# Performance work log

Measured on AMD Instinct MI355X. Metric: run time of the kernel, lower is better.

The kernel has to match this reference:

```python
import jax, jax.numpy as jnp
import numpy as np

N = 40000      # nodes
E = 640000     # edges
D = 128        # in_dim == hidden_dim
G = 64         # graphs in batch
L = 3          # n_layers
EPS = 1e-5     # BatchNorm eps


def setup_inputs() -> dict:
    key = jax.random.key(0)
    ks = jax.random.split(key, 8)
    x = jax.random.normal(ks[0], (N, D), dtype=jnp.float32)
    edge_index = jax.random.randint(ks[1], (2, E), 0, N, dtype=jnp.int64)
    batch = jnp.sort(jax.random.randint(ks[2], (N,), 0, G, dtype=jnp.int64))
    Ws = jax.random.normal(ks[3], (L, D, D), dtype=jnp.float32) * 0.05
    bs = jnp.zeros((L, D), jnp.float32)
    gammas = jnp.ones((L, D), jnp.float32)
    betas = jnp.zeros((L, D), jnp.float32)
    w1 = jax.random.normal(ks[4], (D, D // 2), dtype=jnp.float32) * 0.05
    b1 = jnp.zeros((D // 2,), jnp.float32)
    w2 = jax.random.normal(ks[5], (D // 2, 1), dtype=jnp.float32) * 0.05
    b2 = jnp.zeros((1,), jnp.float32)
    return {"x": x, "edge_index": edge_index, "batch": batch, "Ws": Ws,
            "bs": bs, "gammas": gammas, "betas": betas,
            "w1": w1, "b1": b1, "w2": w2, "b2": b2}


def reference(x, edge_index, batch, Ws, bs, gammas, betas, w1, b1, w2, b2):
    # GCNConv (PyG default): add self-loops, symmetric D^-1/2 (A+I) D^-1/2 norm
    loops = jnp.arange(N, dtype=edge_index.dtype)
    src = jnp.concatenate([edge_index[0], loops])  # [E+N]
    dst = jnp.concatenate([edge_index[1], loops])  # [E+N]
    deg = jax.ops.segment_sum(jnp.ones_like(dst, dtype=x.dtype), dst, num_segments=N)
    dinv = jnp.where(deg > 0, jax.lax.rsqrt(deg), 0.0)
    norm = (dinv[src] * dinv[dst])[:, None]        # [E+N, 1]

    h = x
    for l in range(L):
        h = h @ Ws[l] + bs[l]                                  # linear transform
        h = jax.ops.segment_sum(h[src] * norm, dst, num_segments=N)  # scatter-add agg
        h = jax.nn.relu(h)
        # BatchNorm1d (training-mode batch statistics, biased var)
        mean = h.mean(axis=0)
        var = h.var(axis=0)
        h = gammas[l] * (h - mean) * jax.lax.rsqrt(var + EPS) + betas[l]
        # dropout p=0.0 -> identity

    # global_mean_pool over graph ids
    counts = jax.ops.segment_sum(jnp.ones((N,), h.dtype), batch, num_segments=G)
    pooled = jax.ops.segment_sum(h, batch, num_segments=G) / jnp.maximum(counts, 1.0)[:, None]

    out = jax.nn.relu(pooled @ w1 + b1) @ w2 + b2
    return out.squeeze(-1)  # [G]
```

## Files before the change

kernel.cpp:

```cpp
#include <hip/hip_runtime.h>
#include <hip/hip_fp16.h>

#define N_NODES 40000
#define N_EDGES 640000
#define DIM 128
#define N_GRAPHS 64
#define BN_EPS 1e-5f
#define AGG_BLOCKS 2048
#define SCAN_NB 40
#define GEMM_NB (N_NODES / 64)
#define WTP 136

typedef _Float16 f16x8 __attribute__((ext_vector_type(8)));
typedef float    f32x4 __attribute__((ext_vector_type(4)));

__global__ __launch_bounds__(256) void k_count_edges(const int* __restrict__ ei, int* __restrict__ cnt,
                                                     int* __restrict__ rank) {
    int e = blockIdx.x * 256 + threadIdx.x;
    if (e < N_EDGES) rank[e] = atomicAdd(&cnt[ei[N_EDGES + e]], 1);
}

__global__ __launch_bounds__(1024) void k_scan_blk(const int* __restrict__ cnt, int* __restrict__ off,
                                                   int* __restrict__ blocksum) {
    __shared__ int sums[1024];
    int i = blockIdx.x * 1024 + threadIdx.x;
    int v = (i < N_NODES) ? cnt[i] : 0;
    sums[threadIdx.x] = v;
    __syncthreads();
    for (int d = 1; d < 1024; d <<= 1) {
        int t = (threadIdx.x >= d) ? sums[threadIdx.x - d] : 0;
        __syncthreads();
        sums[threadIdx.x] += t;
        __syncthreads();
    }
    if (i < N_NODES) off[i] = sums[threadIdx.x] - v;
    if (threadIdx.x == 1023) blocksum[blockIdx.x] = sums[1023];
}

__global__ __launch_bounds__(1024) void k_scan_fix(const int* __restrict__ cnt, const int* __restrict__ blocksum,
                                                   int* __restrict__ off, float* __restrict__ dinv,
                                                   const int* __restrict__ batch, int* __restrict__ goff) {
    __shared__ int bo[2];
    if (threadIdx.x == 0) {
        int run = 0, tot = 0;
        for (int b = 0; b < SCAN_NB; ++b) {
            int v = blocksum[b];
            if (b < (int)blockIdx.x) run += v;
            tot += v;
        }
        bo[0] = run; bo[1] = tot;
    }
    __syncthreads();
    int i = blockIdx.x * 1024 + threadIdx.x;
    if (i < N_NODES) {
        off[i] += bo[0];
        dinv[i] = rsqrtf((float)(cnt[i] + 1));
        int b = batch[i];
        int bp = (i == 0) ? -1 : batch[i - 1];
        for (int g = bp + 1; g <= b; ++g) goff[g] = i;
        if (i == N_NODES - 1)
            for (int g = b + 1; g <= N_GRAPHS; ++g) goff[g] = N_NODES;
    }
    if (i == 0) off[N_NODES] = bo[1];
}

__global__ __launch_bounds__(256) void k_fill(const int* __restrict__ ei, const int* __restrict__ rank,
                                              const int* __restrict__ off, int* __restrict__ elist) {
    int e = blockIdx.x * 256 + threadIdx.x;
    if (e < N_EDGES) {
        int s = ei[e];
        int d = ei[N_EDGES + e];
        elist[off[d] + rank[e]] = s;
    }
}

__global__ __launch_bounds__(256) void k_prepw(const float* __restrict__ Ws, __half* __restrict__ wt) {
    int idx = blockIdx.x * 256 + threadIdx.x;
    if (idx >= 3 * DIM * DIM) return;
    int l = idx >> 14;
    int rem = idx & 16383;
    int k = rem >> 7;
    int c = rem & 127;
    float w = Ws[(size_t)l * DIM * DIM + k * DIM + c];
    __half hi = __float2half(w);
    __half lo = __float2half(w - __half2float(hi));
    size_t base = (size_t)l * 2 * DIM * WTP;
    wt[base + (size_t)c * WTP + k] = hi;
    wt[base + (size_t)DIM * WTP + (size_t)c * WTP + k] = lo;
}

__device__ __forceinline__ void gemm_core(const __half* __restrict__ wt2, const float* __restrict__ bias,
                                          __half* __restrict__ out16, __half* Wl2, __half* Al,
                                          int t, long row0) {
    {
        const float4* src = (const float4*)wt2;
        float4* dst = (float4*)Wl2;
        for (int i = t; i < 4352; i += 256) dst[i] = src[i];
    }
    __syncthreads();

    int w = t >> 6;
    int l = t & 63;
    int lr = l & 15;
    int lk = (l >> 4) * 8;

    f32x4 acc[8];
#pragma unroll
    for (int i = 0; i < 8; ++i) acc[i] = (f32x4)(0.f);

#pragma unroll
    for (int ks = 0; ks < 4; ++ks) {
        f16x8 a = *(const f16x8*)&Al[(w * 16 + lr) * WTP + ks * 32 + lk];
#pragma unroll
        for (int tile = 0; tile < 8; ++tile) {
            f16x8 bh = *(const f16x8*)&Wl2[(tile * 16 + lr) * WTP + ks * 32 + lk];
            f16x8 bl = *(const f16x8*)&Wl2[DIM * WTP + (tile * 16 + lr) * WTP + ks * 32 + lk];
            acc[tile] = __builtin_amdgcn_mfma_f32_16x16x32_f16(a, bh, acc[tile], 0, 0, 0);
            acc[tile] = __builtin_amdgcn_mfma_f32_16x16x32_f16(a, bl, acc[tile], 0, 0, 0);
        }
    }

    long orow = row0 + w * 16 + (l >> 4) * 4;
#pragma unroll
    for (int tile = 0; tile < 8; ++tile) {
        int col = tile * 16 + lr;
        float b = bias[col];
#pragma unroll
        for (int i = 0; i < 4; ++i)
            out16[(orow + i) * DIM + col] = __float2half(acc[tile][i] + b);
    }
}

__global__ __launch_bounds__(256) void k_gemm_f32(const float* __restrict__ in, const __half* __restrict__ wt2,
                                                  const float* __restrict__ bias, __half* __restrict__ out16) {
    __shared__ __half Wl2[2 * DIM * WTP];
    __shared__ __half Al[64 * WTP];
    int t = threadIdx.x;
    long row0 = (long)blockIdx.x * 64;
    for (int i = t; i < 2048; i += 256) {
        int r = i >> 5, k4 = i & 31;
        float4 v = ((const float4*)(in + (row0 + r) * DIM))[k4];
        __half2* d = (__half2*)&Al[r * WTP + k4 * 4];
        d[0] = __floats2half2_rn(v.x, v.y);
        d[1] = __floats2half2_rn(v.z, v.w);
    }
    gemm_core(wt2, bias, out16, Wl2, Al, t, row0);
}

__global__ __launch_bounds__(256) void k_gemm_f16(const __half* __restrict__ in, const __half* __restrict__ wt2,
                                                  const float* __restrict__ bias, const float* __restrict__ ac,
                                                  __half* __restrict__ out16) {
    __shared__ __half Wl2[2 * DIM * WTP];
    __shared__ __half Al[64 * WTP];
    int t = threadIdx.x;
    long row0 = (long)blockIdx.x * 64;
    for (int i = t; i < 1024; i += 256) {
        int r = i >> 4, k8 = i & 15;
        const __half2* src = (const __half2*)(in + (row0 + r) * DIM + k8 * 8);
        int k = k8 * 8;
        float2 f0 = __half22float2(src[0]);
        float2 f1 = __half22float2(src[1]);
        float2 f2 = __half22float2(src[2]);
        float2 f3 = __half22float2(src[3]);
        f0.x = fmaf(ac[k + 0], f0.x, ac[DIM + k + 0]); f0.y = fmaf(ac[k + 1], f0.y, ac[DIM + k + 1]);
        f1.x = fmaf(ac[k + 2], f1.x, ac[DIM + k + 2]); f1.y = fmaf(ac[k + 3], f1.y, ac[DIM + k + 3]);
        f2.x = fmaf(ac[k + 4], f2.x, ac[DIM + k + 4]); f2.y = fmaf(ac[k + 5], f2.y, ac[DIM + k + 5]);
        f3.x = fmaf(ac[k + 6], f3.x, ac[DIM + k + 6]); f3.y = fmaf(ac[k + 7], f3.y, ac[DIM + k + 7]);
        __half2* d = (__half2*)&Al[r * WTP + k];
        d[0] = __floats2half2_rn(f0.x, f0.y);
        d[1] = __floats2half2_rn(f1.x, f1.y);
        d[2] = __floats2half2_rn(f2.x, f2.y);
        d[3] = __floats2half2_rn(f3.x, f3.y);
    }
    gemm_core(wt2, bias, out16, Wl2, Al, t, row0);
}

__global__ __launch_bounds__(256) void k_agg(const __half* __restrict__ h16, const int* __restrict__ off,
                                             const int* __restrict__ elist,
                                             const float* __restrict__ dinv, __half* __restrict__ hout,
                                             float* __restrict__ partials) {
    __shared__ float colacc[256];
    colacc[threadIdx.x] = 0.f;
    __syncthreads();

    const __half2* rows = (const __half2*)h16;
    int lane = threadIdx.x & 63;
    int wid = (blockIdx.x * 256 + threadIdx.x) >> 6;
    const int NW = AGG_BLOCKS * 4;
    float s0 = 0.f, s1 = 0.f, q0 = 0.f, q1 = 0.f;

    for (int i = wid; i < N_NODES; i += NW) {
        float di = dinv[i];
        float selfc = di * di;
        float2 rv = __half22float2(rows[(long)i * 64 + lane]);
        float a0 = rv.x * selfc, a1 = rv.y * selfc;
        int e  = off[i];
        int e1 = off[i + 1];
#pragma unroll 4
        for (; e < e1; ++e) {
            int s = elist[e];
            float c = dinv[s] * di;
            float2 r = __half22float2(rows[(long)s * 64 + lane]);
            a0 = fmaf(r.x, c, a0);
            a1 = fmaf(r.y, c, a1);
        }
        a0 = fmaxf(a0, 0.f);
        a1 = fmaxf(a1, 0.f);
        ((__half2*)(hout + (long)i * DIM))[lane] = __floats2half2_rn(a0, a1);
        s0 += a0; q0 += a0 * a0; s1 += a1; q1 += a1 * a1;
    }

    atomicAdd(&colacc[2 * lane],           s0);
    atomicAdd(&colacc[2 * lane + 1],       s1);
    atomicAdd(&colacc[128 + 2 * lane],     q0);
    atomicAdd(&colacc[128 + 2 * lane + 1], q1);
    __syncthreads();
    partials[(long)blockIdx.x * 256 + threadIdx.x] = colacc[threadIdx.x];
}

__global__ __launch_bounds__(1024) void k_stats(const float* __restrict__ partials,
                                                const float* __restrict__ gamma, const float* __restrict__ beta,
                                                float* __restrict__ ac) {
    __shared__ float ls[1024], lq[1024];
    int dd = threadIdx.x & 15;
    int seg = threadIdx.x >> 4;
    int d = blockIdx.x * 16 + dd;
    float s = 0.f, q = 0.f;
    for (int b = seg; b < AGG_BLOCKS; b += 64) {
        s += partials[b * 256 + d];
        q += partials[b * 256 + 128 + d];
    }
    ls[threadIdx.x] = s; lq[threadIdx.x] = q;
    __syncthreads();
    for (int off = 512; off >= 16; off >>= 1) {
        if (threadIdx.x < off) {
            ls[threadIdx.x] += ls[threadIdx.x + off];
            lq[threadIdx.x] += lq[threadIdx.x + off];
        }
        __syncthreads();
    }
    if (threadIdx.x < 16) {
        s = ls[threadIdx.x]; q = lq[threadIdx.x];
        float mean = s * (1.f / N_NODES);
        float var  = q * (1.f / N_NODES) - mean * mean;
        float a = gamma[d] * rsqrtf(var + BN_EPS);
        ac[d] = a;
        ac[DIM + d] = fmaf(-mean, a, beta[d]);
    }
}

__global__ __launch_bounds__(1024) void k_pool(const __half* __restrict__ h, const float* __restrict__ ac,
                                               const int* __restrict__ goff, float* __restrict__ pooled) {
    __shared__ float2 red[1024];
    int g = blockIdx.x;
    int d2 = threadIdx.x & 63;
    int seg = threadIdx.x >> 6;
    int r0 = goff[g], r1 = goff[g + 1];
    const __half2* rows = (const __half2*)h;
    float s0 = 0.f, s1 = 0.f;
    for (int r = r0 + seg; r < r1; r += 16) {
        float2 v = __half22float2(rows[(long)r * 64 + d2]);
        s0 += v.x; s1 += v.y;
    }
    red[threadIdx.x] = make_float2(s0, s1);
    __syncthreads();
    for (int off = 512; off >= 64; off >>= 1) {
        if (threadIdx.x < off) {
            red[threadIdx.x].x += red[threadIdx.x + off].x;
            red[threadIdx.x].y += red[threadIdx.x + off].y;
        }
        __syncthreads();
    }
    if (threadIdx.x < 64) {
        float2 s = red[threadIdx.x];
        int n = r1 - r0;
        float fn = (float)n;
        float denom = (float)(n > 0 ? n : 1);
        int d = 2 * threadIdx.x;
        pooled[g * DIM + d]     = (ac[d] * s.x     + ac[DIM + d] * fn)     / denom;
        pooled[g * DIM + d + 1] = (ac[d + 1] * s.y + ac[DIM + d + 1] * fn) / denom;
    }
}

__global__ __launch_bounds__(64) void k_mlp(const float* __restrict__ pooled, const float* __restrict__ w1,
                                            const float* __restrict__ b1, const float* __restrict__ w2,
                                            const float* __restrict__ b2, float* __restrict__ out) {
    int g = blockIdx.x, j = threadIdx.x;
    const float* p = pooled + g * DIM;
    float h = b1[j];
#pragma unroll
    for (int k = 0; k < DIM; ++k) h = fmaf(p[k], w1[k * 64 + j], h);
    h = fmaxf(h, 0.f);
    float v = h * w2[j];
#pragma unroll
    for (int o = 32; o > 0; o >>= 1) v += __shfl_down(v, o);
    if (j == 0) out[g] = v + b2[0];
}

extern "C" void kernel_launch(void* const* d_in, const int* in_sizes, int n_in,
                              void* d_out, int out_size, void* d_ws, size_t ws_size,
                              hipStream_t stream) {
    const float* x      = (const float*)d_in[0];
    const int*   ei     = (const int*)d_in[1];
    const int*   batch  = (const int*)d_in[2];
    const float* Ws     = (const float*)d_in[3];
    const float* bs     = (const float*)d_in[4];
    const float* gammas = (const float*)d_in[5];
    const float* betas  = (const float*)d_in[6];
    const float* w1     = (const float*)d_in[7];
    const float* b1     = (const float*)d_in[8];
    const float* w2     = (const float*)d_in[9];
    const float* b2     = (const float*)d_in[10];
    float* out = (float*)d_out;

    char* p = (char*)d_ws;
    auto alloc = [&](size_t bytes) { void* r = (void*)p; p += (bytes + 255) & ~(size_t)255; return r; };
    int*    cnt      = (int*)alloc((size_t)N_NODES * 4);
    int*    off      = (int*)alloc((size_t)(N_NODES + 1) * 4);
    int*    rank     = (int*)alloc((size_t)N_EDGES * 4);
    int*    goff     = (int*)alloc((size_t)(N_GRAPHS + 1) * 4);
    int*    blocksum = (int*)alloc((size_t)(SCAN_NB + 1) * 4);
    int*    elist    = (int*)alloc((size_t)N_EDGES * 4);
    float*  dinv     = (float*)alloc((size_t)N_NODES * 4);
    __half* wt       = (__half*)alloc((size_t)3 * 2 * DIM * WTP * 2);
    __half* h16      = (__half*)alloc((size_t)N_NODES * DIM * 2);
    __half* v16      = (__half*)alloc((size_t)N_NODES * DIM * 2);
    float*  parts    = (float*)alloc((size_t)AGG_BLOCKS * 256 * 4);
    float*  ac       = (float*)alloc(256 * 4);
    float*  pooled   = (float*)alloc((size_t)N_GRAPHS * DIM * 4);

    hipMemsetAsync(cnt, 0, (size_t)N_NODES * 4, stream);

    k_count_edges<<<(N_EDGES + 255) / 256, 256, 0, stream>>>(ei, cnt, rank);
    k_scan_blk<<<SCAN_NB, 1024, 0, stream>>>(cnt, off, blocksum);
    k_scan_fix<<<SCAN_NB, 1024, 0, stream>>>(cnt, blocksum, off, dinv, batch, goff);
    k_fill<<<(N_EDGES + 255) / 256, 256, 0, stream>>>(ei, rank, off, elist);
    k_prepw<<<(3 * DIM * DIM + 255) / 256, 256, 0, stream>>>(Ws, wt);

    for (int l = 0; l < 3; ++l) {
        if (l == 0)
            k_gemm_f32<<<GEMM_NB, 256, 0, stream>>>(x, wt, bs, h16);
        else
            k_gemm_f16<<<GEMM_NB, 256, 0, stream>>>(v16, wt + (size_t)l * 2 * DIM * WTP,
                                                    bs + (size_t)l * DIM, ac, h16);
        k_agg<<<AGG_BLOCKS, 256, 0, stream>>>(h16, off, elist, dinv, v16, parts);
        k_stats<<<8, 1024, 0, stream>>>(parts, gammas + (size_t)l * DIM, betas + (size_t)l * DIM, ac);
    }
    k_pool<<<N_GRAPHS, 1024, 0, stream>>>(v16, ac, goff, pooled);
    k_mlp<<<N_GRAPHS, 64, 0, stream>>>(pooled, w1, b1, w2, b2, out);
}
```

Baseline: 276.3 us.

## Make GEMM persistent with double-buffered A tiles and fuse pool with MLP

The GEMM kernels become persistent: 256 blocks each load the split-fp16 weight matrix into LDS once and loop over 64-row tiles. The next A tile is staged into a second LDS buffer while MFMA runs on the current one. This amortizes the 70KB weight copy per block and overlaps global loads with compute, at the cost of more LDS per block (lower occupancy) and fewer blocks than the 256 CUs might prefer. Separately, the pooling and MLP head are fused into one kernel, which removes a launch and the pooled buffer round trip.

After: 260.4 us. 5.7% less time.

```diff
diff --git a/kernel.cpp b/kernel.cpp
--- a/kernel.cpp
+++ b/kernel.cpp
@@ -8,7 +8,8 @@
 #define BN_EPS 1e-5f
 #define AGG_BLOCKS 2048
 #define SCAN_NB 40
-#define GEMM_NB (N_NODES / 64)
+#define NTILES 625
+#define GEMM_BLOCKS 256
 #define WTP 136
 
 typedef _Float16 f16x8 __attribute__((ext_vector_type(8)));
@@ -89,54 +90,7 @@
     wt[base + (size_t)DIM * WTP + (size_t)c * WTP + k] = lo;
 }
 
-__device__ __forceinline__ void gemm_core(const __half* __restrict__ wt2, const float* __restrict__ bias,
-                                          __half* __restrict__ out16, __half* Wl2, __half* Al,
-                                          int t, long row0) {
-    {
-        const float4* src = (const float4*)wt2;
-        float4* dst = (float4*)Wl2;
-        for (int i = t; i < 4352; i += 256) dst[i] = src[i];
-    }
-    __syncthreads();
-
-    int w = t >> 6;
-    int l = t & 63;
-    int lr = l & 15;
-    int lk = (l >> 4) * 8;
-
-    f32x4 acc[8];
-#pragma unroll
-    for (int i = 0; i < 8; ++i) acc[i] = (f32x4)(0.f);
-
-#pragma unroll
-    for (int ks = 0; ks < 4; ++ks) {
-        f16x8 a = *(const f16x8*)&Al[(w * 16 + lr) * WTP + ks * 32 + lk];
-#pragma unroll
-        for (int tile = 0; tile < 8; ++tile) {
-            f16x8 bh = *(const f16x8*)&Wl2[(tile * 16 + lr) * WTP + ks * 32 + lk];
-            f16x8 bl = *(const f16x8*)&Wl2[DIM * WTP + (tile * 16 + lr) * WTP + ks * 32 + lk];
-            acc[tile] = __builtin_amdgcn_mfma_f32_16x16x32_f16(a, bh, acc[tile], 0, 0, 0);
-            acc[tile] = __builtin_amdgcn_mfma_f32_16x16x32_f16(a, bl, acc[tile], 0, 0, 0);
-        }
-    }
-
-    long orow = row0 + w * 16 + (l >> 4) * 4;
-#pragma unroll
-    for (int tile = 0; tile < 8; ++tile) {
-        int col = tile * 16 + lr;
-        float b = bias[col];
-#pragma unroll
-        for (int i = 0; i < 4; ++i)
-            out16[(orow + i) * DIM + col] = __float2half(acc[tile][i] + b);
-    }
-}
-
-__global__ __launch_bounds__(256) void k_gemm_f32(const float* __restrict__ in, const __half* __restrict__ wt2,
-                                                  const float* __restrict__ bias, __half* __restrict__ out16) {
-    __shared__ __half Wl2[2 * DIM * WTP];
-    __shared__ __half Al[64 * WTP];
-    int t = threadIdx.x;
-    long row0 = (long)blockIdx.x * 64;
+__device__ __forceinline__ void stage_a_f32(const float* __restrict__ in, __half* Al, long row0, int t) {
     for (int i = t; i < 2048; i += 256) {
         int r = i >> 5, k4 = i & 31;
         float4 v = ((const float4*)(in + (row0 + r) * DIM))[k4];
@@ -144,16 +98,10 @@
         d[0] = __floats2half2_rn(v.x, v.y);
         d[1] = __floats2half2_rn(v.z, v.w);
     }
-    gemm_core(wt2, bias, out16, Wl2, Al, t, row0);
-}
-
-__global__ __launch_bounds__(256) void k_gemm_f16(const __half* __restrict__ in, const __half* __restrict__ wt2,
-                                                  const float* __restrict__ bias, const float* __restrict__ ac,
-                                                  __half* __restrict__ out16) {
-    __shared__ __half Wl2[2 * DIM * WTP];
-    __shared__ __half Al[64 * WTP];
-    int t = threadIdx.x;
-    long row0 = (long)blockIdx.x * 64;
+}
+
+__device__ __forceinline__ void stage_a_f16(const __half* __restrict__ in, const float* __restrict__ ac,
+                                            __half* Al, long row0, int t) {
     for (int i = t; i < 1024; i += 256) {
         int r = i >> 4, k8 = i & 15;
         const __half2* src = (const __half2*)(in + (row0 + r) * DIM + k8 * 8);
@@ -172,7 +120,90 @@
         d[2] = __floats2half2_rn(f2.x, f2.y);
         d[3] = __floats2half2_rn(f3.x, f3.y);
     }
-    gemm_core(wt2, bias, out16, Wl2, Al, t, row0);
+}
+
+__device__ __forceinline__ void compute_tile(const __half* Wl2, const __half* Al,
+                                             const float* __restrict__ bias, __half* __restrict__ out16,
+                                             int t, long row0) {
+    int w = t >> 6;
+    int l = t & 63;
+    int lr = l & 15;
+    int lk = (l >> 4) * 8;
+
+    f32x4 acc[8];
+#pragma unroll
+    for (int i = 0; i < 8; ++i) acc[i] = (f32x4)(0.f);
+
+#pragma unroll
+    for (int ks = 0; ks < 4; ++ks) {
+        f16x8 a = *(const f16x8*)&Al[(w * 16 + lr) * WTP + ks * 32 + lk];
+#pragma unroll
+        for (int tile = 0; tile < 8; ++tile) {
+            f16x8 bh = *(const f16x8*)&Wl2[(tile * 16 + lr) * WTP + ks * 32 + lk];
+            f16x8 bl = *(const f16x8*)&Wl2[DIM * WTP + (tile * 16 + lr) * WTP + ks * 32 + lk];
+            acc[tile] = __builtin_amdgcn_mfma_f32_16x16x32_f16(a, bh, acc[tile], 0, 0, 0);
+            acc[tile] = __builtin_amdgcn_mfma_f32_16x16x32_f16(a, bl, acc[tile], 0, 0, 0);
+        }
+    }
+
+    long orow = row0 + w * 16 + (l >> 4) * 4;
+#pragma unroll
+    for (int tile = 0; tile < 8; ++tile) {
+        int col = tile * 16 + lr;
+        float b = bias[col];
+#pragma unroll
+        for (int i = 0; i < 4; ++i)
+            out16[(orow + i) * DIM + col] = __float2half(acc[tile][i] + b);
+    }
+}
+
+__global__ __launch_bounds__(256) void k_gemm_f32(const float* __restrict__ in, const __half* __restrict__ wt2,
+                                                  const float* __restrict__ bias, __half* __restrict__ out16) {
+    __shared__ __half Wl2[2 * DIM * WTP];
+    __shared__ __half Al[2][64 * WTP];
+    int t = threadIdx.x;
+    {
+        const float4* src = (const float4*)wt2;
+        float4* dst = (float4*)Wl2;
+        for (int i = t; i < 4352; i += 256) dst[i] = src[i];
+    }
+    int tile = blockIdx.x;
+    stage_a_f32(in, Al[0], (long)tile * 64, t);
+    __syncthreads();
+    int buf = 0;
+    while (tile < NTILES) {
+        int next = tile + GEMM_BLOCKS;
+        if (next < NTILES) stage_a_f32(in, Al[buf ^ 1], (long)next * 64, t);
+        compute_tile(Wl2, Al[buf], bias, out16, t, (long)tile * 64);
+        __syncthreads();
+        buf ^= 1;
+        tile = next;
+    }
+}
+
+__global__ __launch_bounds__(256) void k_gemm_f16(const __half* __restrict__ in, const __half* __restrict__ wt2,
+                                                  const float* __restrict__ bias, const float* __restrict__ ac,
+                                                  __half* __restrict__ out16) {
+    __shared__ __half Wl2[2 * DIM * WTP];
+    __shared__ __half Al[2][64 * WTP];
+    int t = threadIdx.x;
+    {
+        const float4* src = (const float4*)wt2;
+        float4* dst = (float4*)Wl2;
+        for (int i = t; i < 4352; i += 256) dst[i] = src[i];
+    }
+    int tile = blockIdx.x;
+    stage_a_f16(in, ac, Al[0], (long)tile * 64, t);
+    __syncthreads();
+    int buf = 0;
+    while (tile < NTILES) {
+        int next = tile + GEMM_BLOCKS;
+        if (next < NTILES) stage_a_f16(in, ac, Al[buf ^ 1], (long)next * 64, t);
+        compute_tile(Wl2, Al[buf], bias, out16, t, (long)tile * 64);
+        __syncthreads();
+        buf ^= 1;
+        tile = next;
+    }
 }
 
 __global__ __launch_bounds__(256) void k_agg(const __half* __restrict__ h16, const int* __restrict__ off,
@@ -249,9 +280,13 @@
     }
 }
 
-__global__ __launch_bounds__(1024) void k_pool(const __half* __restrict__ h, const float* __restrict__ ac,
-                                               const int* __restrict__ goff, float* __restrict__ pooled) {
+__global__ __launch_bounds__(1024) void k_poolmlp(const __half* __restrict__ h, const float* __restrict__ ac,
+                                                  const int* __restrict__ goff,
+                                                  const float* __restrict__ w1, const float* __restrict__ b1,
+                                                  const float* __restrict__ w2, const float* __restrict__ b2,
+                                                  float* __restrict__ out) {
     __shared__ float2 red[1024];
+    __shared__ float pl[DIM];
     int g = blockIdx.x;
     int d2 = threadIdx.x & 63;
     int seg = threadIdx.x >> 6;
@@ -277,24 +312,21 @@
         float fn = (float)n;
         float denom = (float)(n > 0 ? n : 1);
         int d = 2 * threadIdx.x;
-        pooled[g * DIM + d]     = (ac[d] * s.x     + ac[DIM + d] * fn)     / denom;
-        pooled[g * DIM + d + 1] = (ac[d + 1] * s.y + ac[DIM + d + 1] * fn) / denom;
-    }
-}
-
-__global__ __launch_bounds__(64) void k_mlp(const float* __restrict__ pooled, const float* __restrict__ w1,
-                                            const float* __restrict__ b1, const float* __restrict__ w2,
-                                            const float* __restrict__ b2, float* __restrict__ out) {
-    int g = blockIdx.x, j = threadIdx.x;
-    const float* p = pooled + g * DIM;
-    float h = b1[j];
-#pragma unroll
-    for (int k = 0; k < DIM; ++k) h = fmaf(p[k], w1[k * 64 + j], h);
-    h = fmaxf(h, 0.f);
-    float v = h * w2[j];
-#pragma unroll
-    for (int o = 32; o > 0; o >>= 1) v += __shfl_down(v, o);
-    if (j == 0) out[g] = v + b2[0];
+        pl[d]     = (ac[d] * s.x     + ac[DIM + d] * fn)     / denom;
+        pl[d + 1] = (ac[d + 1] * s.y + ac[DIM + d + 1] * fn) / denom;
+    }
+    __syncthreads();
+    if (threadIdx.x < 64) {
+        int j = threadIdx.x;
+        float hh = b1[j];
+#pragma unroll
+        for (int k = 0; k < DIM; ++k) hh = fmaf(pl[k], w1[k * 64 + j], hh);
+        hh = fmaxf(hh, 0.f);
+        float v = hh * w2[j];
+#pragma unroll
+        for (int o = 32; o > 0; o >>= 1) v += __shfl_down(v, o);
+        if (j == 0) out[g] = v + b2[0];
+    }
 }
 
 extern "C" void kernel_launch(void* const* d_in, const int* in_sizes, int n_in,
@@ -327,7 +359,6 @@
     __half* v16      = (__half*)alloc((size_t)N_NODES * DIM * 2);
     float*  parts    = (float*)alloc((size_t)AGG_BLOCKS * 256 * 4);
     float*  ac       = (float*)alloc(256 * 4);
-    float*  pooled   = (float*)alloc((size_t)N_GRAPHS * DIM * 4);
 
     hipMemsetAsync(cnt, 0, (size_t)N_NODES * 4, stream);
 
@@ -339,13 +370,12 @@
 
     for (int l = 0; l < 3; ++l) {
         if (l == 0)
-            k_gemm_f32<<<GEMM_NB, 256, 0, stream>>>(x, wt, bs, h16);
+            k_gemm_f32<<<GEMM_BLOCKS, 256, 0, stream>>>(x, wt, bs, h16);
         else
-            k_gemm_f16<<<GEMM_NB, 256, 0, stream>>>(v16, wt + (size_t)l * 2 * DIM * WTP,
-                                                    bs + (size_t)l * DIM, ac, h16);
+            k_gemm_f16<<<GEMM_BLOCKS, 256, 0, stream>>>(v16, wt + (size_t)l * 2 * DIM * WTP,
+                                                        bs + (size_t)l * DIM, ac, h16);
         k_agg<<<AGG_BLOCKS, 256, 0, stream>>>(h16, off, elist, dinv, v16, parts);
         k_stats<<<8, 1024, 0, stream>>>(parts, gammas + (size_t)l * DIM, betas + (size_t)l * DIM, ac);
     }
-    k_pool<<<N_GRAPHS, 1024, 0, stream>>>(v16, ac, goff, pooled);
-    k_mlp<<<N_GRAPHS, 64, 0, stream>>>(pooled, w1, b1, w2, b2, out);
-}
+    k_poolmlp<<<N_GRAPHS, 1024, 0, stream>>>(v16, ac, goff, w1, b1, w2, b2, out);
+}
```
